# Kernel tuning notes

Hardware: AMD Instinct MI355X
Metric: run time of the kernel (lower is better)

## Reference

```python
import jax, jax.numpy as jnp
import numpy as np

N = 50000
E = 800000
IN_C = 128
OUT_C = 128
HEADS = 8
BASES = 4
N_AGG = 4  # symadd, mean, max, std
HEAD_D = OUT_C // HEADS  # 16


def setup_inputs() -> dict:
    key = jax.random.key(0)
    k1, k2, k3, k4, k5 = jax.random.split(key, 5)
    x = jax.random.normal(k1, (N, IN_C), dtype=jnp.float32)
    edge_index = jax.random.randint(k2, (2, E), 0, N, dtype=jnp.int64)
    # glorot for each basis weight [IN_C, HEAD_D]
    glorot_scale = np.sqrt(6.0 / (IN_C + HEAD_D))
    bases_W = jax.random.uniform(k3, (BASES, IN_C, HEAD_D), dtype=jnp.float32,
                                 minval=-glorot_scale, maxval=glorot_scale)
    # comb_weights Linear(IN_C, HEADS*BASES*N_AGG), kaiming-uniform-ish init
    fan = IN_C
    lim = np.sqrt(1.0 / fan)
    comb_W = jax.random.uniform(k4, (IN_C, HEADS * BASES * N_AGG), dtype=jnp.float32,
                                minval=-lim, maxval=lim)
    comb_b = jax.random.uniform(k5, (HEADS * BASES * N_AGG,), dtype=jnp.float32,
                                minval=-lim, maxval=lim)
    bias = jnp.zeros((OUT_C,), dtype=jnp.float32)
    return {"x": x, "edge_index": edge_index, "bases_W": bases_W,
            "comb_W": comb_W, "comb_b": comb_b, "bias": bias}


def _egc_forward(x, edge_index, bases_W, comb_W, comb_b, bias):
    n = x.shape[0]
    row, col = edge_index[0], edge_index[1]  # messages flow row -> col
    # bases: [N, BASES, HEAD_D] -> [N, BASES*HEAD_D]
    bases = jnp.einsum('nc,bcd->nbd', x, bases_W).reshape(n, BASES * HEAD_D)
    msgs = bases[row]  # [E, BASES*HEAD_D]
    ones_e = jnp.ones((row.shape[0],), dtype=x.dtype)
    cnt = jax.ops.segment_sum(ones_e, col, num_segments=n)  # in-degree
    cnt_c = jnp.maximum(cnt, 1.0)[:, None]
    # --- symadd: gcn_norm with self-loops, weighted sum ---
    loops = jnp.arange(n, dtype=row.dtype)
    row_sl = jnp.concatenate([row, loops])
    col_sl = jnp.concatenate([col, loops])
    deg = jax.ops.segment_sum(jnp.ones((row_sl.shape[0],), dtype=x.dtype), col_sl,
                              num_segments=n)
    dinv = jnp.where(deg > 0, jax.lax.rsqrt(deg), 0.0)
    norm = dinv[row_sl] * dinv[col_sl]  # [E+N]
    symadd = jax.ops.segment_sum(norm[:, None] * bases[row_sl], col_sl,
                                 num_segments=n)
    # --- mean ---
    s = jax.ops.segment_sum(msgs, col, num_segments=n)
    mean = s / cnt_c
    # --- max (torch_scatter fills empty segments with 0) ---
    mx = jax.ops.segment_max(msgs, col, num_segments=n)
    mx = jnp.where(cnt[:, None] > 0, mx, 0.0)
    # --- std: sqrt(relu(E[m^2]-E[m]^2)+1e-5) ---
    mean_sq = jax.ops.segment_sum(msgs * msgs, col, num_segments=n) / cnt_c
    var = mean_sq - mean * mean
    std = jnp.sqrt(jax.nn.relu(var) + 1e-5)
    # stack aggregators: each [N, BASES, HEAD_D] -> [N, BASES, N_AGG, HEAD_D]
    aggs = jnp.stack([a.reshape(n, BASES, HEAD_D) for a in (symadd, mean, mx, std)],
                     axis=2)
    # combination weights with softmax over (BASES*N_AGG)
    w = x @ comb_W + comb_b  # [N, HEADS*BASES*N_AGG]
    w = jax.nn.softmax(w.reshape(n, HEADS, BASES * N_AGG), axis=-1)
    w = w.reshape(n, HEADS, BASES, N_AGG)
    # z[n,h,d] = sum_{b,a} w[n,h,b,a] * aggs[n,b,a,d]
    z = jnp.einsum('nhba,nbad->nhd', w, aggs).reshape(n, OUT_C)
    return z + bias


def reference(x, edge_index, bases_W, comb_W, comb_b, bias):
    return _egc_forward(x, edge_index, bases_W, comb_W, comb_b, bias)
```

## Files before the change

### kernel.cpp

```cpp
#include <hip/hip_runtime.h>
#include <math.h>

#define IN_C 128
#define OUT_C 128
#define BD 64
#define SLOTS 48

__device__ __forceinline__ uint32_t f2bf(float f) {
    uint32_t u = __float_as_uint(f);
    return (u + 0x7fffu + ((u >> 16) & 1u)) >> 16;
}

__global__ void k_place(const int* __restrict__ row, const int* __restrict__ col,
                        int E, int* __restrict__ cnt, int* __restrict__ esrc) {
    int e = blockIdx.x * blockDim.x + threadIdx.x;
    if (e < E) {
        int c = col[e];
        int p = atomicAdd(&cnt[c], 1);
        if (p < SLOTS) esrc[c * SLOTS + p] = row[e];
    }
}

__global__ void k_bases(const float* __restrict__ x, const float* __restrict__ Wb,
                        const int* __restrict__ cnt, uint32_t* __restrict__ bases16,
                        float* __restrict__ dinv, int Nn) {
    __shared__ float xs[4][IN_C];
    int t = threadIdx.x;
    int nb = blockIdx.x * 4;
    for (int i = t; i < 4 * IN_C; i += 256) {
        int r = i >> 7, c = i & 127;
        int n = nb + r;
        xs[r][c] = (n < Nn) ? x[(size_t)n * IN_C + c] : 0.f;
    }
    __syncthreads();
    int nl = t >> 6, dout = t & 63;
    int n = nb + nl;
    if (n >= Nn) return;
    int b = dout >> 4, d = dout & 15;
    const float* wp = Wb + b * (IN_C * 16) + d;
    float acc = 0.f;
#pragma unroll 8
    for (int c = 0; c < IN_C; ++c) acc = fmaf(xs[nl][c], wp[c * 16], acc);
    float other = __shfl(acc, dout ^ 1, 64);
    if (!(dout & 1)) {
        uint32_t lo = f2bf(acc), hi = f2bf(other);
        bases16[(size_t)n * 32 + (dout >> 1)] = (hi << 16) | lo;
    }
    if (dout == 0) dinv[n] = rsqrtf((float)cnt[n] + 1.0f);
}

__global__ void k_fused(const float* __restrict__ x, const uint32_t* __restrict__ bu,
                        const float* __restrict__ dinv, const int* __restrict__ cnt,
                        const int* __restrict__ esrc, const float* __restrict__ Wc,
                        const float* __restrict__ bc, const float* __restrict__ bias,
                        float* __restrict__ out, int Nn) {
    __shared__ float xs[4][IN_C];
    __shared__ float wsh[4][128];
    __shared__ float agg[4][4][BD];
    int t = threadIdx.x;
    int wv = t >> 6, lane = t & 63;
    int node = (blockIdx.x << 2) + wv;
    bool valid = node < Nn;
    int sub = lane & 31;

    const float* xr = x + (size_t)node * IN_C;
    xs[wv][lane]      = valid ? xr[lane] : 0.f;
    xs[wv][lane + 64] = valid ? xr[lane + 64] : 0.f;
    __syncthreads();

    float l0 = bc[lane], l1 = bc[lane + 64];
#pragma unroll 4
    for (int c = 0; c < IN_C; ++c) {
        float xc = xs[wv][c];
        l0 = fmaf(xc, Wc[(size_t)c * 128 + lane], l0);
        l1 = fmaf(xc, Wc[(size_t)c * 128 + lane + 64], l1);
    }
    float m0 = l0, m1 = l1;
#pragma unroll
    for (int m = 1; m < 16; m <<= 1) {
        m0 = fmaxf(m0, __shfl_xor(m0, m, 64));
        m1 = fmaxf(m1, __shfl_xor(m1, m, 64));
    }
    float e0 = __expf(l0 - m0), e1 = __expf(l1 - m1);
    float s0l = e0, s1l = e1;
#pragma unroll
    for (int m = 1; m < 16; m <<= 1) {
        s0l += __shfl_xor(s0l, m, 64);
        s1l += __shfl_xor(s1l, m, 64);
    }
    wsh[wv][lane]      = e0 / s0l;
    wsh[wv][lane + 64] = e1 / s1l;

    int cf = valid ? cnt[node] : 0;
    int c = min(cf, SLOTS);
    int src_l = 0; float dv_l = 0.f;
    if (valid && lane < c) {
        src_l = esrc[node * SLOTS + lane];
        dv_l = dinv[src_l];
    }
    float s0 = 0.f, s1 = 0.f, q0 = 0.f, q1 = 0.f, y0 = 0.f, y1 = 0.f;
    float x0 = -INFINITY, x1 = -INFINITY;
#pragma unroll 4
    for (int j = 0; j < c; ++j) {
        int src = __shfl(src_l, j, 64);
        float dv = __shfl(dv_l, j, 64);
        uint32_t u = bu[(size_t)src * 32 + sub];
        float f0 = __uint_as_float(u << 16);
        float f1 = __uint_as_float(u & 0xffff0000u);
        s0 += f0;                 s1 += f1;
        q0 = fmaf(f0, f0, q0);    q1 = fmaf(f1, f1, q1);
        y0 = fmaf(dv, f0, y0);    y1 = fmaf(dv, f1, y1);
        x0 = fmaxf(x0, f0);       x1 = fmaxf(x1, f1);
    }

    if (valid && lane < 32) {
        float dn = dinv[node];
        uint32_t us = bu[(size_t)node * 32 + sub];
        float b0 = __uint_as_float(us << 16);
        float b1 = __uint_as_float(us & 0xffff0000u);
        float cc = fmaxf((float)cf, 1.0f);
        int f = sub << 1;
        agg[wv][0][f]     = fmaf(dn * dn, b0, dn * y0);
        agg[wv][0][f + 1] = fmaf(dn * dn, b1, dn * y1);
        float mean0 = s0 / cc, mean1 = s1 / cc;
        agg[wv][1][f]     = mean0;
        agg[wv][1][f + 1] = mean1;
        agg[wv][2][f]     = (cf > 0) ? x0 : 0.f;
        agg[wv][2][f + 1] = (cf > 0) ? x1 : 0.f;
        agg[wv][3][f]     = sqrtf(fmaxf(q0 / cc - mean0 * mean0, 0.f) + 1e-5f);
        agg[wv][3][f + 1] = sqrtf(fmaxf(q1 / cc - mean1 * mean1, 0.f) + 1e-5f);
    }
    __syncthreads();

    if (valid) {
        float* outp = out + (size_t)node * OUT_C;
#pragma unroll
        for (int hf = 0; hf < 2; ++hf) {
            int o = lane + (hf << 6);
            int h = o >> 4, d = o & 15;
            float z = bias[o];
#pragma unroll
            for (int b = 0; b < 4; ++b) {
                const float* wp = &wsh[wv][h * 16 + b * 4];
                z = fmaf(wp[0], agg[wv][0][b * 16 + d], z);
                z = fmaf(wp[1], agg[wv][1][b * 16 + d], z);
                z = fmaf(wp[2], agg[wv][2][b * 16 + d], z);
                z = fmaf(wp[3], agg[wv][3][b * 16 + d], z);
            }
            outp[o] = z;
        }
    }
}

extern "C" void kernel_launch(void* const* d_in, const int* in_sizes, int n_in,
                              void* d_out, int out_size, void* d_ws, size_t ws_size,
                              hipStream_t stream) {
    const float* x       = (const float*)d_in[0];
    const int* ei        = (const int*)d_in[1];
    const float* bases_W = (const float*)d_in[2];
    const float* comb_W  = (const float*)d_in[3];
    const float* comb_b  = (const float*)d_in[4];
    const float* bias    = (const float*)d_in[5];
    float* out = (float*)d_out;

    int N = in_sizes[0] / IN_C;
    int E = in_sizes[1] / 2;
    const int* row = ei;
    const int* col = ei + E;

    char* ws = (char*)d_ws;
    size_t off = 0;
    auto alloc = [&](size_t bytes) {
        void* p = ws + off;
        off = (off + bytes + 255) & ~(size_t)255;
        return p;
    };
    int*      cnt     = (int*)alloc((size_t)N * 4);
    float*    dinv    = (float*)alloc((size_t)N * 4);
    int*      esrc    = (int*)alloc((size_t)N * SLOTS * 4);
    uint32_t* bases16 = (uint32_t*)alloc((size_t)N * 32 * 4);

    if (off > ws_size) return;

    hipMemsetAsync(cnt, 0, (size_t)N * 4, stream);

    int eb = (E + 255) / 256;
    k_place<<<eb, 256, 0, stream>>>(row, col, E, cnt, esrc);
    k_bases<<<(N + 3) / 4, 256, 0, stream>>>(x, bases_W, cnt, bases16, dinv, N);
    k_fused<<<(N + 3) / 4, 256, 0, stream>>>(x, bases16, dinv, cnt, esrc, comb_W,
                                             comb_b, bias, out, N);
}
```

Before: 317.4 us.

## Transpose comb weights for vectorized dot, split wave halves across neighbor edges

Adds a small kernel that transposes comb_W so each lane can read its weight row as float4 and compute the softmax logits with vectorized loads and two independent accumulator chains. The neighbor gather loop now assigns two edges per iteration, one to each half of the wave, so all 64 lanes load instead of 32 duplicating work. The halves are then merged with cross-half shuffles. This halves the gather iterations, but the per-lane strided row reads of WcT are uncoalesced, and one extra launch and a workspace buffer are added.

```diff
diff --git a/kernel.cpp b/kernel.cpp
--- a/kernel.cpp
+++ b/kernel.cpp
@@ -18,6 +18,14 @@
         int c = col[e];
         int p = atomicAdd(&cnt[c], 1);
         if (p < SLOTS) esrc[c * SLOTS + p] = row[e];
+    }
+}
+
+__global__ void k_wct(const float* __restrict__ Wc, float* __restrict__ WcT) {
+    int i = blockIdx.x * 256 + threadIdx.x;
+    if (i < 128 * 128) {
+        int c = i >> 7, o = i & 127;
+        WcT[o * 128 + c] = Wc[i];
     }
 }
 
@@ -51,7 +59,7 @@
 
 __global__ void k_fused(const float* __restrict__ x, const uint32_t* __restrict__ bu,
                         const float* __restrict__ dinv, const int* __restrict__ cnt,
-                        const int* __restrict__ esrc, const float* __restrict__ Wc,
+                        const int* __restrict__ esrc, const float* __restrict__ WcT,
                         const float* __restrict__ bc, const float* __restrict__ bias,
                         float* __restrict__ out, int Nn) {
     __shared__ float xs[4][IN_C];
@@ -61,35 +69,46 @@
     int wv = t >> 6, lane = t & 63;
     int node = (blockIdx.x << 2) + wv;
     bool valid = node < Nn;
-    int sub = lane & 31;
+    int sub = lane & 31, half = lane >> 5;
 
     const float* xr = x + (size_t)node * IN_C;
     xs[wv][lane]      = valid ? xr[lane] : 0.f;
     xs[wv][lane + 64] = valid ? xr[lane + 64] : 0.f;
     __syncthreads();
 
-    float l0 = bc[lane], l1 = bc[lane + 64];
-#pragma unroll 4
-    for (int c = 0; c < IN_C; ++c) {
-        float xc = xs[wv][c];
-        l0 = fmaf(xc, Wc[(size_t)c * 128 + lane], l0);
-        l1 = fmaf(xc, Wc[(size_t)c * 128 + lane + 64], l1);
-    }
-    float m0 = l0, m1 = l1;
-#pragma unroll
-    for (int m = 1; m < 16; m <<= 1) {
-        m0 = fmaxf(m0, __shfl_xor(m0, m, 64));
-        m1 = fmaxf(m1, __shfl_xor(m1, m, 64));
-    }
-    float e0 = __expf(l0 - m0), e1 = __expf(l1 - m1);
-    float s0l = e0, s1l = e1;
-#pragma unroll
-    for (int m = 1; m < 16; m <<= 1) {
-        s0l += __shfl_xor(s0l, m, 64);
-        s1l += __shfl_xor(s1l, m, 64);
-    }
-    wsh[wv][lane]      = e0 / s0l;
-    wsh[wv][lane + 64] = e1 / s1l;
+    {
+        const float4* w0 = (const float4*)(WcT + (size_t)lane * IN_C);
+        const float4* w1 = (const float4*)(WcT + (size_t)(lane + 64) * IN_C);
+        const float4* xv = (const float4*)xs[wv];
+        float l0a = 0.f, l0b = 0.f, l1a = 0.f, l1b = 0.f;
+#pragma unroll
+        for (int k = 0; k < 32; k += 2) {
+            float4 xk0 = xv[k], xk1 = xv[k + 1];
+            float4 a0 = w0[k], a1 = w0[k + 1];
+            float4 b0 = w1[k], b1 = w1[k + 1];
+            l0a = fmaf(xk0.x, a0.x, fmaf(xk0.y, a0.y, fmaf(xk0.z, a0.z, fmaf(xk0.w, a0.w, l0a))));
+            l0b = fmaf(xk1.x, a1.x, fmaf(xk1.y, a1.y, fmaf(xk1.z, a1.z, fmaf(xk1.w, a1.w, l0b))));
+            l1a = fmaf(xk0.x, b0.x, fmaf(xk0.y, b0.y, fmaf(xk0.z, b0.z, fmaf(xk0.w, b0.w, l1a))));
+            l1b = fmaf(xk1.x, b1.x, fmaf(xk1.y, b1.y, fmaf(xk1.z, b1.z, fmaf(xk1.w, b1.w, l1b))));
+        }
+        float l0 = bc[lane] + l0a + l0b;
+        float l1 = bc[lane + 64] + l1a + l1b;
+        float m0 = l0, m1 = l1;
+#pragma unroll
+        for (int m = 1; m < 16; m <<= 1) {
+            m0 = fmaxf(m0, __shfl_xor(m0, m, 64));
+            m1 = fmaxf(m1, __shfl_xor(m1, m, 64));
+        }
+        float e0 = __expf(l0 - m0), e1 = __expf(l1 - m1);
+        float s0l = e0, s1l = e1;
+#pragma unroll
+        for (int m = 1; m < 16; m <<= 1) {
+            s0l += __shfl_xor(s0l, m, 64);
+            s1l += __shfl_xor(s1l, m, 64);
+        }
+        wsh[wv][lane]      = e0 / s0l;
+        wsh[wv][lane + 64] = e1 / s1l;
+    }
 
     int cf = valid ? cnt[node] : 0;
     int c = min(cf, SLOTS);
@@ -100,10 +119,28 @@
     }
     float s0 = 0.f, s1 = 0.f, q0 = 0.f, q1 = 0.f, y0 = 0.f, y1 = 0.f;
     float x0 = -INFINITY, x1 = -INFINITY;
-#pragma unroll 4
-    for (int j = 0; j < c; ++j) {
-        int src = __shfl(src_l, j, 64);
-        float dv = __shfl(dv_l, j, 64);
+    if (c & 1) {
+        int src = __shfl(src_l, 0, 64);
+        float dv = __shfl(dv_l, 0, 64);
+        uint32_t u = bu[(size_t)src * 32 + sub];
+        float f0 = __uint_as_float(u << 16);
+        float f1 = __uint_as_float(u & 0xffff0000u);
+        bool lo = (half == 0);
+        float g0 = lo ? f0 : 0.f, g1 = lo ? f1 : 0.f, dz = lo ? dv : 0.f;
+        s0 += g0; s1 += g1;
+        q0 = fmaf(g0, g0, q0); q1 = fmaf(g1, g1, q1);
+        y0 = fmaf(dz, g0, y0); y1 = fmaf(dz, g1, y1);
+        x0 = lo ? fmaxf(x0, f0) : x0;
+        x1 = lo ? fmaxf(x1, f1) : x1;
+    }
+#pragma unroll 2
+    for (int j = (c & 1); j < c; j += 2) {
+        int sA = __shfl(src_l, j, 64);
+        int sB = __shfl(src_l, j + 1, 64);
+        float dA = __shfl(dv_l, j, 64);
+        float dB = __shfl(dv_l, j + 1, 64);
+        int src = half ? sB : sA;
+        float dv = half ? dB : dA;
         uint32_t u = bu[(size_t)src * 32 + sub];
         float f0 = __uint_as_float(u << 16);
         float f1 = __uint_as_float(u & 0xffff0000u);
@@ -112,6 +149,11 @@
         y0 = fmaf(dv, f0, y0);    y1 = fmaf(dv, f1, y1);
         x0 = fmaxf(x0, f0);       x1 = fmaxf(x1, f1);
     }
+    s0 += __shfl(s0, sub + 32, 64);  s1 += __shfl(s1, sub + 32, 64);
+    q0 += __shfl(q0, sub + 32, 64);  q1 += __shfl(q1, sub + 32, 64);
+    y0 += __shfl(y0, sub + 32, 64);  y1 += __shfl(y1, sub + 32, 64);
+    x0 = fmaxf(x0, __shfl(x0, sub + 32, 64));
+    x1 = fmaxf(x1, __shfl(x1, sub + 32, 64));
 
     if (valid && lane < 32) {
         float dn = dinv[node];
@@ -179,6 +221,7 @@
     float*    dinv    = (float*)alloc((size_t)N * 4);
     int*      esrc    = (int*)alloc((size_t)N * SLOTS * 4);
     uint32_t* bases16 = (uint32_t*)alloc((size_t)N * 32 * 4);
+    float*    WcT     = (float*)alloc(128 * 128 * 4);
 
     if (off > ws_size) return;
 
@@ -186,7 +229,8 @@
 
     int eb = (E + 255) / 256;
     k_place<<<eb, 256, 0, stream>>>(row, col, E, cnt, esrc);
+    k_wct<<<64, 256, 0, stream>>>(comb_W, WcT);
     k_bases<<<(N + 3) / 4, 256, 0, stream>>>(x, bases_W, cnt, bases16, dinv, N);
-    k_fused<<<(N + 3) / 4, 256, 0, stream>>>(x, bases16, dinv, cnt, esrc, comb_W,
+    k_fused<<<(N + 3) / 4, 256, 0, stream>>>(x, bases16, dinv, cnt, esrc, WcT,
                                              comb_b, bias, out, N);
 }
```

Result: slower. 600.1 us (+89.0%).
